# Kernel optimization log

Hardware: AMD Instinct MI355X
Metric: run time of the kernel (lower is better)

Reference implementation:

```python
import jax, jax.numpy as jnp
import numpy as np

MAX_PATH_DISTANCE = 5


def setup_inputs() -> dict:
    key = jax.random.key(0)
    k1, k2, k3, k4, k5 = jax.random.split(key, 5)
    N = 8192
    E = 4_000_000
    x = jax.random.normal(k1, (N, 128), dtype=jnp.float32)
    src = jax.random.randint(k2, (E,), 0, N, dtype=jnp.int64)
    dst = jax.random.randint(k3, (E,), 0, N, dtype=jnp.int64)
    # path lengths; original computes len(paths[src][dst]) >= 1
    path_len = jax.random.randint(k4, (E,), 0, 6, dtype=jnp.int64)
    # learned parameter b of shape [max_path_distance]
    b = jax.random.normal(k5, (MAX_PATH_DISTANCE,), dtype=jnp.float32)
    return {"x": x, "b": b, "src": src, "dst": dst, "path_len": path_len}


def reference(x, b, src, dst, path_len):
    N = x.shape[0]
    # index = min(len, max_path_distance) - 1, clamped to valid range
    idx = jnp.clip(path_len, 1, MAX_PATH_DISTANCE) - 1  # [E]
    vals = b[idx]  # [E] gather from tiny table
    spatial = jnp.zeros((N, N), dtype=b.dtype)
    spatial = spatial.at[src, dst].set(vals)  # scatter into pairwise bias matrix
    return spatial
```

## Files before the change

kernel.cpp:

```cpp
#include <hip/hip_runtime.h>

#define MAX_PATH_DISTANCE 5
#define NROW 8192
#define ROWS_PER_BKT 128
#define NBKT 64
#define SLICES 17
#define EPB 4096
#define CAPB (SLICES * EPB)
#define CAPR 768
#define BLK 256


__device__ __forceinline__ int clamp_bidx(int pl) {
    int c = pl < 1 ? 1 : (pl > MAX_PATH_DISTANCE ? MAX_PATH_DISTANCE : pl);
    return c - 1;
}

__global__ __launch_bounds__(BLK) void se_coarse(
        const int* __restrict__ src, const int* __restrict__ dst,
        const int* __restrict__ plen,
        unsigned long long* __restrict__ bkt,
        unsigned int* __restrict__ bkt_cur, int E) {
    __shared__ unsigned long long stage[EPB];
    __shared__ unsigned int hist[NBKT], base_l[NBKT], cur[NBKT], gbase[NBKT];
    const int tid = threadIdx.x;
    const int e0  = blockIdx.x * EPB;

    if (tid < NBKT) { hist[tid] = 0u; cur[tid] = 0u; }
    __syncthreads();

    unsigned long long ent[16];
    int bk[16];
#pragma unroll
    for (int j = 0; j < 16; ++j) {
        int e = e0 + j * BLK + tid;
        bk[j] = -1;
        if (e < E) {
            int s = src[e], d = dst[e], p = plen[e];
            unsigned int key = ((unsigned int)(e + 1) << 3)
                             | (unsigned int)clamp_bidx(p);
            ent[j] = ((unsigned long long)(unsigned int)s << 38)
                   | ((unsigned long long)(unsigned int)d << 25)
                   | (unsigned long long)key;
            bk[j] = s >> 7;
            atomicAdd(&hist[bk[j]], 1u);
        }
    }
    __syncthreads();

    if (tid == 0) {
        unsigned int run = 0;
        for (int i = 0; i < NBKT; ++i) { base_l[i] = run; run += hist[i]; }
    }
    __syncthreads();

    if (tid < NBKT) gbase[tid] = atomicAdd(&bkt_cur[tid], hist[tid]);

#pragma unroll
    for (int j = 0; j < 16; ++j) {
        if (bk[j] >= 0) {
            unsigned int p = atomicAdd(&cur[bk[j]], 1u);
            stage[base_l[bk[j]] + p] = ent[j];
        }
    }
    __syncthreads();

    const int total = (int)(base_l[NBKT - 1] + hist[NBKT - 1]);
    for (int i = tid; i < total; i += BLK) {
        unsigned long long v = stage[i];
        unsigned int s  = (unsigned int)(v >> 38);
        unsigned int bb = s >> 7;
        unsigned int pos = gbase[bb] + ((unsigned int)i - base_l[bb]);
        if (pos < CAPB) bkt[(size_t)bb * CAPB + pos] = v;
    }
}

__global__ __launch_bounds__(BLK) void se_fine(
        const unsigned long long* __restrict__ bkt,
        const unsigned int* __restrict__ bkt_cur,
        unsigned long long* __restrict__ rbins,
        unsigned int* __restrict__ rcur) {
    __shared__ unsigned long long stage[EPB];
    __shared__ unsigned int hist[ROWS_PER_BKT], base_l[ROWS_PER_BKT],
                            cur[ROWS_PER_BKT], gbase[ROWS_PER_BKT];
    const int tid = threadIdx.x;
    const int b   = blockIdx.x / SLICES;
    const int sl  = blockIdx.x % SLICES;

    unsigned int cnt = bkt_cur[b]; if (cnt > CAPB) cnt = CAPB;
    const int i0 = sl * EPB;
    int n = (int)cnt - i0;
    if (n <= 0) return;
    if (n > EPB) n = EPB;

    if (tid < ROWS_PER_BKT) { hist[tid] = 0u; cur[tid] = 0u; }
    __syncthreads();

    const unsigned long long* bp = bkt + (size_t)b * CAPB + i0;
    unsigned long long ent[16];
    int rl[16];
#pragma unroll
    for (int j = 0; j < 16; ++j) {
        int i = j * BLK + tid;
        rl[j] = -1;
        if (i < n) {
            unsigned long long v = bp[i];
            ent[j] = v;
            rl[j]  = (int)((v >> 38) & 127u);
            atomicAdd(&hist[rl[j]], 1u);
        }
    }
    __syncthreads();

    if (tid == 0) {
        unsigned int run = 0;
        for (int i = 0; i < ROWS_PER_BKT; ++i) { base_l[i] = run; run += hist[i]; }
    }
    __syncthreads();

    if (tid < ROWS_PER_BKT)
        gbase[tid] = atomicAdd(&rcur[b * ROWS_PER_BKT + tid], hist[tid]);

#pragma unroll
    for (int j = 0; j < 16; ++j) {
        if (rl[j] >= 0) {
            unsigned int p = atomicAdd(&cur[rl[j]], 1u);
            stage[base_l[rl[j]] + p] = ent[j];
        }
    }
    __syncthreads();

    for (int i = tid; i < n; i += BLK) {
        unsigned long long v = stage[i];
        unsigned int s   = (unsigned int)((v >> 38) & 0x1FFFu);
        unsigned int r_l = s & 127u;
        unsigned int pos = gbase[r_l] + ((unsigned int)i - base_l[r_l]);
        if (pos < CAPR) rbins[(size_t)s * CAPR + pos] = v;
    }
}

__global__ __launch_bounds__(BLK) void se_rows(
        const unsigned long long* __restrict__ rbins,
        const unsigned int* __restrict__ rcur,
        const float* __restrict__ b,
        float* __restrict__ out) {
    __shared__ unsigned int lds[NROW];
    const int r = blockIdx.x, tid = threadIdx.x;

    for (int i = tid; i < NROW; i += BLK) lds[i] = 0u;
    __syncthreads();

    unsigned int cnt = rcur[r]; if (cnt > CAPR) cnt = CAPR;
    const unsigned long long* bp = rbins + (size_t)r * CAPR;

    for (unsigned int i = tid; i < cnt; i += BLK) {
        unsigned long long v = bp[i];
        atomicMax(&lds[(unsigned int)((v >> 25) & 0x1FFFu)],
                  (unsigned int)(v & 0x1FFFFFFu));
    }
    __syncthreads();

    for (unsigned int i = tid; i < cnt; i += BLK) {
        unsigned long long v = bp[i];
        unsigned int key = (unsigned int)(v & 0x1FFFFFFu);
        unsigned int d   = (unsigned int)((v >> 25) & 0x1FFFu);
        if (lds[d] == key) lds[d] = __float_as_uint(b[key & 7u]);
    }
    __syncthreads();

    float4* out4 = reinterpret_cast<float4*>(out + (size_t)r * NROW);
    const float4* l4 = reinterpret_cast<const float4*>(lds);
    for (int k = tid; k < NROW / 4; k += BLK) out4[k] = l4[k];
}


__global__ void se_scatter_keys(const int* __restrict__ src,
                                const int* __restrict__ dst,
                                const int* __restrict__ plen,
                                unsigned int* __restrict__ out,
                                int E, int N) {
    int e = blockIdx.x * blockDim.x + threadIdx.x;
    if (e >= E) return;
    unsigned int key = ((unsigned int)(e + 1) << 3)
                     | (unsigned int)clamp_bidx(plen[e]);
    atomicMax(&out[(size_t)src[e] * (size_t)N + (size_t)dst[e]], key);
}

__global__ void se_resolve(const int* __restrict__ src,
                           const int* __restrict__ dst,
                           const int* __restrict__ plen,
                           const float* __restrict__ b,
                           unsigned int* __restrict__ out,
                           int E, int N) {
    int e = blockIdx.x * blockDim.x + threadIdx.x;
    if (e >= E) return;
    unsigned int key = ((unsigned int)(e + 1) << 3)
                     | (unsigned int)clamp_bidx(plen[e]);
    size_t off = (size_t)src[e] * (size_t)N + (size_t)dst[e];
    if (out[off] == key) {
        reinterpret_cast<float*>(out)[off] = b[key & 7u];
    }
}


extern "C" void kernel_launch(void* const* d_in, const int* in_sizes, int n_in,
                              void* d_out, int out_size, void* d_ws, size_t ws_size,
                              hipStream_t stream) {
    const float* b    = (const float*)d_in[1];
    const int*   src  = (const int*)d_in[2];
    const int*   dst  = (const int*)d_in[3];
    const int*   plen = (const int*)d_in[4];

    const int N = in_sizes[0] / 128;
    const int E = in_sizes[2];

    const size_t rbins_bytes = (size_t)NROW * CAPR * sizeof(unsigned long long);
    const size_t bkt_bytes   = (size_t)NBKT * CAPB * sizeof(unsigned long long);
    const size_t rcur_bytes  = (size_t)NROW * sizeof(unsigned int);
    const size_t bcur_bytes  = (size_t)NBKT * sizeof(unsigned int);
    const size_t need = rbins_bytes + bkt_bytes + rcur_bytes + bcur_bytes;

    const int block = 256;
    const int gridE = (E + block - 1) / block;

    if (N == NROW && (unsigned int)E < (1u << 22) && ws_size >= need) {
        unsigned long long* rbins = (unsigned long long*)d_ws;
        unsigned long long* bktp  = (unsigned long long*)((char*)d_ws + rbins_bytes);
        unsigned int* rcur  = (unsigned int*)((char*)d_ws + rbins_bytes + bkt_bytes);
        unsigned int* bcur  = (unsigned int*)((char*)rcur + rcur_bytes);

        hipMemsetAsync(rcur, 0, rcur_bytes + bcur_bytes, stream);
        se_coarse<<<(E + EPB - 1) / EPB, BLK, 0, stream>>>(src, dst, plen,
                                                           bktp, bcur, E);
        se_fine<<<NBKT * SLICES, BLK, 0, stream>>>(bktp, bcur, rbins, rcur);
        se_rows<<<NROW, BLK, 0, stream>>>(rbins, rcur, b, (float*)d_out);
    } else {
        hipMemsetAsync(d_out, 0, (size_t)out_size * sizeof(float), stream);
        se_scatter_keys<<<gridE, block, 0, stream>>>(src, dst, plen,
                                                     (unsigned int*)d_out, E, N);
        se_resolve<<<gridE, block, 0, stream>>>(src, dst, plen, b,
                                                (unsigned int*)d_out, E, N);
    }
}
```

Before: 119.0 us.

## Use per-wave histograms, vectorized int4 loads, and register-cached row entries

The coarse pass now loads src/dst/path_len as int4 vectors, four edges per thread. The coarse and fine bucketing kernels keep a histogram per wave and build per-wave base offsets, so the second LDS atomic pass needs no separate cursor array and contends less across waves. The row kernel loads its entries into registers once and reuses them for the max and resolve passes instead of reading global memory twice. It also overlaps those loads with LDS zeroing. The fast path now requires E to be divisible by 4, and a zero entry is used as the empty sentinel. Edge e=0 never encodes to zero because its key includes e+1.

Result: no change. 118.0 us (-0.9%).

```diff
diff --git a/kernel.cpp b/kernel.cpp
--- a/kernel.cpp
+++ b/kernel.cpp
@@ -9,6 +9,7 @@
 #define CAPB (SLICES * EPB)
 #define CAPR 768
 #define BLK 256
+#define NWAVE 4
 
 
 __device__ __forceinline__ int clamp_bidx(int pl) {
@@ -17,60 +18,86 @@
 }
 
 __global__ __launch_bounds__(BLK) void se_coarse(
-        const int* __restrict__ src, const int* __restrict__ dst,
-        const int* __restrict__ plen,
+        const int4* __restrict__ src4, const int4* __restrict__ dst4,
+        const int4* __restrict__ plen4,
         unsigned long long* __restrict__ bkt,
-        unsigned int* __restrict__ bkt_cur, int E) {
+        unsigned int* __restrict__ bkt_cur, int E4) {
     __shared__ unsigned long long stage[EPB];
-    __shared__ unsigned int hist[NBKT], base_l[NBKT], cur[NBKT], gbase[NBKT];
+    __shared__ unsigned int hist[NWAVE][NBKT], wbase[NWAVE][NBKT];
+    __shared__ unsigned int base_l[NBKT], gbase[NBKT], s_total;
     const int tid = threadIdx.x;
-    const int e0  = blockIdx.x * EPB;
-
-    if (tid < NBKT) { hist[tid] = 0u; cur[tid] = 0u; }
+    const int w   = tid >> 6;
+    const int q0  = blockIdx.x * (EPB / 4);
+
+    for (int i = tid; i < NWAVE * NBKT; i += BLK)
+        ((unsigned int*)hist)[i] = 0u;
     __syncthreads();
 
     unsigned long long ent[16];
-    int bk[16];
-#pragma unroll
-    for (int j = 0; j < 16; ++j) {
-        int e = e0 + j * BLK + tid;
-        bk[j] = -1;
-        if (e < E) {
-            int s = src[e], d = dst[e], p = plen[e];
-            unsigned int key = ((unsigned int)(e + 1) << 3)
-                             | (unsigned int)clamp_bidx(p);
-            ent[j] = ((unsigned long long)(unsigned int)s << 38)
-                   | ((unsigned long long)(unsigned int)d << 25)
-                   | (unsigned long long)key;
-            bk[j] = s >> 7;
-            atomicAdd(&hist[bk[j]], 1u);
-        }
-    }
-    __syncthreads();
-
+#pragma unroll
+    for (int g = 0; g < 4; ++g) {
+        int q = q0 + g * BLK + tid;
+        if (q < E4) {
+            int4 s = src4[q], d = dst4[q], p = plen4[q];
+            int ss[4] = {s.x, s.y, s.z, s.w};
+            int dd[4] = {d.x, d.y, d.z, d.w};
+            int pp[4] = {p.x, p.y, p.z, p.w};
+#pragma unroll
+            for (int c = 0; c < 4; ++c) {
+                int e = q * 4 + c;
+                unsigned int key = ((unsigned int)(e + 1) << 3)
+                                 | (unsigned int)clamp_bidx(pp[c]);
+                unsigned long long v =
+                      ((unsigned long long)(unsigned int)ss[c] << 38)
+                    | ((unsigned long long)(unsigned int)dd[c] << 25)
+                    | (unsigned long long)key;
+                ent[g * 4 + c] = v;
+                atomicAdd(&hist[w][(unsigned int)(v >> 45)], 1u);
+            }
+        } else {
+#pragma unroll
+            for (int c = 0; c < 4; ++c) ent[g * 4 + c] = 0ull;
+        }
+    }
+    __syncthreads();
+
+    if (tid < NBKT)
+        base_l[tid] = hist[0][tid] + hist[1][tid] + hist[2][tid] + hist[3][tid];
+    __syncthreads();
     if (tid == 0) {
         unsigned int run = 0;
-        for (int i = 0; i < NBKT; ++i) { base_l[i] = run; run += hist[i]; }
-    }
-    __syncthreads();
-
-    if (tid < NBKT) gbase[tid] = atomicAdd(&bkt_cur[tid], hist[tid]);
+        for (int i = 0; i < NBKT; ++i) {
+            unsigned int t = base_l[i]; base_l[i] = run; run += t;
+        }
+        s_total = run;
+    }
+    __syncthreads();
+    if (tid < NBKT) {
+        unsigned int t = base_l[tid];
+        unsigned int tot = 0;
+#pragma unroll
+        for (int ww = 0; ww < NWAVE; ++ww) {
+            wbase[ww][tid] = t; t += hist[ww][tid]; tot += hist[ww][tid];
+        }
+        gbase[tid] = atomicAdd(&bkt_cur[tid], tot);
+    }
+    __syncthreads();
 
 #pragma unroll
     for (int j = 0; j < 16; ++j) {
-        if (bk[j] >= 0) {
-            unsigned int p = atomicAdd(&cur[bk[j]], 1u);
-            stage[base_l[bk[j]] + p] = ent[j];
-        }
-    }
-    __syncthreads();
-
-    const int total = (int)(base_l[NBKT - 1] + hist[NBKT - 1]);
-    for (int i = tid; i < total; i += BLK) {
+        if (ent[j]) {
+            unsigned int bb = (unsigned int)(ent[j] >> 45);
+            unsigned int p  = atomicAdd(&wbase[w][bb], 1u);
+            stage[p] = ent[j];
+        }
+    }
+    __syncthreads();
+
+    const unsigned int total = s_total;
+    for (unsigned int i = tid; i < total; i += BLK) {
         unsigned long long v = stage[i];
-        unsigned int s  = (unsigned int)(v >> 38);
-        unsigned int bb = s >> 7;
-        unsigned int pos = gbase[bb] + ((unsigned int)i - base_l[bb]);
+        unsigned int bb  = (unsigned int)(v >> 45);
+        unsigned int pos = gbase[bb] + (i - base_l[bb]);
         if (pos < CAPB) bkt[(size_t)bb * CAPB + pos] = v;
     }
 }
@@ -81,9 +108,10 @@
         unsigned long long* __restrict__ rbins,
         unsigned int* __restrict__ rcur) {
     __shared__ unsigned long long stage[EPB];
-    __shared__ unsigned int hist[ROWS_PER_BKT], base_l[ROWS_PER_BKT],
-                            cur[ROWS_PER_BKT], gbase[ROWS_PER_BKT];
+    __shared__ unsigned int hist[NWAVE][ROWS_PER_BKT], wbase[NWAVE][ROWS_PER_BKT];
+    __shared__ unsigned int base_l[ROWS_PER_BKT], gbase[ROWS_PER_BKT], s_total;
     const int tid = threadIdx.x;
+    const int w   = tid >> 6;
     const int b   = blockIdx.x / SLICES;
     const int sl  = blockIdx.x % SLICES;
 
@@ -93,48 +121,62 @@
     if (n <= 0) return;
     if (n > EPB) n = EPB;
 
-    if (tid < ROWS_PER_BKT) { hist[tid] = 0u; cur[tid] = 0u; }
+    for (int i = tid; i < NWAVE * ROWS_PER_BKT; i += BLK)
+        ((unsigned int*)hist)[i] = 0u;
     __syncthreads();
 
     const unsigned long long* bp = bkt + (size_t)b * CAPB + i0;
     unsigned long long ent[16];
-    int rl[16];
 #pragma unroll
     for (int j = 0; j < 16; ++j) {
         int i = j * BLK + tid;
-        rl[j] = -1;
+        ent[j] = 0ull;
         if (i < n) {
             unsigned long long v = bp[i];
             ent[j] = v;
-            rl[j]  = (int)((v >> 38) & 127u);
-            atomicAdd(&hist[rl[j]], 1u);
-        }
-    }
-    __syncthreads();
-
+            atomicAdd(&hist[w][(unsigned int)(v >> 38) & 127u], 1u);
+        }
+    }
+    __syncthreads();
+
+    if (tid < ROWS_PER_BKT)
+        base_l[tid] = hist[0][tid] + hist[1][tid] + hist[2][tid] + hist[3][tid];
+    __syncthreads();
     if (tid == 0) {
         unsigned int run = 0;
-        for (int i = 0; i < ROWS_PER_BKT; ++i) { base_l[i] = run; run += hist[i]; }
-    }
-    __syncthreads();
-
-    if (tid < ROWS_PER_BKT)
-        gbase[tid] = atomicAdd(&rcur[b * ROWS_PER_BKT + tid], hist[tid]);
+        for (int i = 0; i < ROWS_PER_BKT; ++i) {
+            unsigned int t = base_l[i]; base_l[i] = run; run += t;
+        }
+        s_total = run;
+    }
+    __syncthreads();
+    if (tid < ROWS_PER_BKT) {
+        unsigned int t = base_l[tid];
+        unsigned int tot = 0;
+#pragma unroll
+        for (int ww = 0; ww < NWAVE; ++ww) {
+            wbase[ww][tid] = t; t += hist[ww][tid]; tot += hist[ww][tid];
+        }
+        gbase[tid] = atomicAdd(&rcur[b * ROWS_PER_BKT + tid], tot);
+    }
+    __syncthreads();
 
 #pragma unroll
     for (int j = 0; j < 16; ++j) {
-        if (rl[j] >= 0) {
-            unsigned int p = atomicAdd(&cur[rl[j]], 1u);
-            stage[base_l[rl[j]] + p] = ent[j];
-        }
-    }
-    __syncthreads();
-
-    for (int i = tid; i < n; i += BLK) {
+        if (ent[j]) {
+            unsigned int rl = (unsigned int)(ent[j] >> 38) & 127u;
+            unsigned int p  = atomicAdd(&wbase[w][rl], 1u);
+            stage[p] = ent[j];
+        }
+    }
+    __syncthreads();
+
+    const unsigned int total = s_total;
+    for (unsigned int i = tid; i < total; i += BLK) {
         unsigned long long v = stage[i];
         unsigned int s   = (unsigned int)((v >> 38) & 0x1FFFu);
-        unsigned int r_l = s & 127u;
-        unsigned int pos = gbase[r_l] + ((unsigned int)i - base_l[r_l]);
+        unsigned int rl  = s & 127u;
+        unsigned int pos = gbase[rl] + (i - base_l[rl]);
         if (pos < CAPR) rbins[(size_t)s * CAPR + pos] = v;
     }
 }
@@ -148,20 +190,24 @@
     const int r = blockIdx.x, tid = threadIdx.x;
 
     for (int i = tid; i < NROW; i += BLK) lds[i] = 0u;
-    __syncthreads();
 
     unsigned int cnt = rcur[r]; if (cnt > CAPR) cnt = CAPR;
     const unsigned long long* bp = rbins + (size_t)r * CAPR;
 
-    for (unsigned int i = tid; i < cnt; i += BLK) {
-        unsigned long long v = bp[i];
+    unsigned long long ev[3];
+    int ne = 0;
+    for (unsigned int i = tid; i < cnt; i += BLK) ev[ne++] = bp[i];
+    __syncthreads();
+
+    for (int k = 0; k < ne; ++k) {
+        unsigned long long v = ev[k];
         atomicMax(&lds[(unsigned int)((v >> 25) & 0x1FFFu)],
                   (unsigned int)(v & 0x1FFFFFFu));
     }
     __syncthreads();
 
-    for (unsigned int i = tid; i < cnt; i += BLK) {
-        unsigned long long v = bp[i];
+    for (int k = 0; k < ne; ++k) {
+        unsigned long long v = ev[k];
         unsigned int key = (unsigned int)(v & 0x1FFFFFFu);
         unsigned int d   = (unsigned int)((v >> 25) & 0x1FFFu);
         if (lds[d] == key) lds[d] = __float_as_uint(b[key & 7u]);
@@ -223,15 +269,17 @@
     const int block = 256;
     const int gridE = (E + block - 1) / block;
 
-    if (N == NROW && (unsigned int)E < (1u << 22) && ws_size >= need) {
+    if (N == NROW && (unsigned int)E < (1u << 22) && (E % 4) == 0 &&
+        ws_size >= need) {
         unsigned long long* rbins = (unsigned long long*)d_ws;
         unsigned long long* bktp  = (unsigned long long*)((char*)d_ws + rbins_bytes);
         unsigned int* rcur  = (unsigned int*)((char*)d_ws + rbins_bytes + bkt_bytes);
-        unsigned int* bcur  = (unsigned int*)((char*)rcur + rcur_bytes);
 
         hipMemsetAsync(rcur, 0, rcur_bytes + bcur_bytes, stream);
-        se_coarse<<<(E + EPB - 1) / EPB, BLK, 0, stream>>>(src, dst, plen,
-                                                           bktp, bcur, E);
+        unsigned int* bcur = rcur + NROW;
+        se_coarse<<<(E + EPB - 1) / EPB, BLK, 0, stream>>>(
+            (const int4*)src, (const int4*)dst, (const int4*)plen,
+            bktp, bcur, E / 4);
         se_fine<<<NBKT * SLICES, BLK, 0, stream>>>(bktp, bcur, rbins, rcur);
         se_rows<<<NROW, BLK, 0, stream>>>(rbins, rcur, b, (float*)d_out);
     } else {
```
